# Performance work log

Measured on AMD Instinct MI355X. Metric: run time of the kernel, lower is better.

Reference implementation:

```python
import jax, jax.numpy as jnp
import numpy as np

EPS_PEN = 1e-05


def _penalty(x):
    return jnp.sqrt(x + EPS_PEN)


def _warp(img, flow):
    """Bilinear warp (Resample2d): sample img at (x+u, y+v), clamped borders.
    img: (B,C,H,W), flow: (B,2,H,W) -> (B,C,H,W)."""
    B, C, H, W = img.shape
    xs = jnp.arange(W, dtype=flow.dtype)[None, None, :]  # (1,1,W)
    ys = jnp.arange(H, dtype=flow.dtype)[None, :, None]  # (1,H,1)
    x = xs + flow[:, 0]  # (B,H,W)
    y = ys + flow[:, 1]
    x0f = jnp.floor(x)
    y0f = jnp.floor(y)
    wx = x - x0f  # bilinear weights
    wy = y - y0f
    x0 = jnp.clip(x0f.astype(jnp.int32), 0, W - 1)
    x1 = jnp.clip(x0 + 1, 0, W - 1)
    y0 = jnp.clip(y0f.astype(jnp.int32), 0, H - 1)
    y1 = jnp.clip(y0 + 1, 0, H - 1)
    img_flat = img.reshape(B, C, H * W)

    def gather(yi, xi):
        idx = (yi * W + xi).reshape(B, 1, H * W)
        idx = jnp.broadcast_to(idx, (B, C, H * W))
        return jnp.take_along_axis(img_flat, idx, axis=2).reshape(B, C, H, W)

    v00 = gather(y0, x0)
    v01 = gather(y0, x1)
    v10 = gather(y1, x0)
    v11 = gather(y1, x1)
    wx = wx[:, None]  # (B,1,H,W)
    wy = wy[:, None]
    return ((1 - wy) * ((1 - wx) * v00 + wx * v01)
            + wy * ((1 - wx) * v10 + wx * v11))


def _energy(flow, img1, img2, alpha=1.0, beta=1.0):
    img2_warp = _warp(img2, flow)
    A = jnp.sum((img1 - img2_warp) ** 2, axis=1)          # (B,H,W)
    data_term = jnp.sum(_penalty(A), axis=(1, 2))          # (B,)
    # conv with kernel_dx == horizontal forward diff per channel; dy vertical
    dx = flow[:, :, :, 1:] - flow[:, :, :, :-1]            # (B,2,H,W-1)
    dy = flow[:, :, 1:, :] - flow[:, :, :-1, :]            # (B,2,H-1,W)
    Bx = jnp.pad(jnp.sum(dx ** 2, axis=1), ((0, 0), (0, 0), (0, 1)))
    By = jnp.pad(jnp.sum(dy ** 2, axis=1), ((0, 0), (0, 1), (0, 0)))
    smooth_term = jnp.sum(_penalty(Bx + By), axis=(1, 2))  # (B,)
    return alpha * data_term + beta * smooth_term


def setup_inputs() -> dict:
    key = jax.random.key(0)
    ks = jax.random.split(key, 6)
    B, H, W = 16, 448, 1024
    mean = jax.random.normal(ks[0], (B, 2, H, W), dtype=jnp.float32)
    log_var = jax.random.normal(ks[1], (B, 2, H, W), dtype=jnp.float32)
    img1 = jax.random.uniform(ks[2], (B, 3, H, W), dtype=jnp.float32)
    img2 = jax.random.uniform(ks[3], (B, 3, H, W), dtype=jnp.float32)
    target = jax.random.normal(ks[4], (B, 2, H, W), dtype=jnp.float32)
    eps = jax.random.normal(ks[5], (B, 2, H, W), dtype=jnp.float32)
    return {"mean": mean, "log_var": log_var, "img1": img1, "img2": img2,
            "target": target, "eps": eps}


def reference(mean, log_var, img1, img2, target, eps):
    # reparam: z = mean + exp(log_var/2) * eps  (eps replaces Normal(0,1).sample)
    flow_sample = mean + jnp.exp(log_var / 2.0) * eps
    elbo = _energy(flow_sample, img1, img2) - jnp.sum(log_var, axis=(1, 2, 3)) / 2.0
    mean_elbo = jnp.mean(elbo)
    # elementwise EPE: L2 norm over flow channels of (mean - target)
    epe = jnp.sqrt(jnp.sum((mean - target) ** 2, axis=1))
    mean_epe = jnp.mean(epe)
    return (mean_elbo, mean_epe)
```

## Files before the change

### kernel.cpp

```cpp
#include <hip/hip_runtime.h>

#define BB 16
#define HH 448
#define WW 1024
constexpr int HW    = HH * WW;
constexpr int NBLK  = BB * HH;
constexpr int NTHR  = 256;
constexpr long long TOTAL = (long long)BB * HW;


struct FlowRaw {
    float m0, m1, l0, l1, e0, e1;
    float dm0, dm1, dl0, dl1, de0, de1;
    float t0, t1;
};

__global__ __launch_bounds__(NTHR) void elbo_main(
    const float* __restrict__ mean, const float* __restrict__ lvar,
    const float* __restrict__ img1, const float* __restrict__ img2,
    const float* __restrict__ target, const float* __restrict__ eps,
    float2* __restrict__ partials)
{
    constexpr int NXCD = 8, CPX = NBLK / NXCD;
    const int wg = (blockIdx.x % NXCD) * CPX + blockIdx.x / NXCD;

    const int b = wg / HH;
    const int y = wg - b * HH;
    const int t = threadIdx.x;

    const int fbase = b * 2 * HW + y * WW;
    const int ibase = b * 3 * HW;
    const bool have_dn = (y + 1) < HH;

    const float* __restrict__ p2c0 = img2 + ibase;
    const float* __restrict__ p2c1 = img2 + ibase + HW;
    const float* __restrict__ p2c2 = img2 + ibase + 2 * HW;

    float se = 0.f;
    float sp = 0.f;

    auto load_raw = [&](int k, FlowRaw& r) {
        const int o = fbase + (k << 8) + t;
        r.m0 = mean[o];   r.m1 = mean[o + HW];
        r.l0 = lvar[o];   r.l1 = lvar[o + HW];
        r.e0 = eps[o];    r.e1 = eps[o + HW];
        r.t0 = target[o]; r.t1 = target[o + HW];
        if (have_dn) {
            r.dm0 = mean[o + WW]; r.dm1 = mean[o + WW + HW];
            r.dl0 = lvar[o + WW]; r.dl1 = lvar[o + WW + HW];
            r.de0 = eps[o + WW];  r.de1 = eps[o + WW + HW];
        } else {
            r.dm0 = r.dm1 = r.dl0 = r.dl1 = r.de0 = r.de1 = 0.f;
        }
    };

    FlowRaw cur, nxt;
    load_raw(0, cur);

    #pragma unroll
    for (int k = 0; k < 4; ++k) {
        if (k < 3) load_raw(k + 1, nxt);

        const int x = (k << 8) + t;
        const int o = fbase + x;

        const float u = cur.m0 + __expf(0.5f * cur.l0) * cur.e0;
        const float v = cur.m1 + __expf(0.5f * cur.l1) * cur.e1;
        float un = 0.f, vn = 0.f;
        if (have_dn) {
            un = cur.dm0 + __expf(0.5f * cur.dl0) * cur.de0;
            vn = cur.dm1 + __expf(0.5f * cur.dl1) * cur.de1;
        }

        {
            const float du = cur.m0 - cur.t0, dv = cur.m1 - cur.t1;
            sp += sqrtf(du * du + dv * dv);
        }
        se -= 0.5f * (cur.l0 + cur.l1);

        float uR = __shfl_down(u, 1);
        float vR = __shfl_down(v, 1);
        if (((t & 63) == 63) && (x + 1 < WW)) {
            const int o1 = o + 1;
            uR = mean[o1]      + __expf(0.5f * lvar[o1])      * eps[o1];
            vR = mean[o1 + HW] + __expf(0.5f * lvar[o1 + HW]) * eps[o1 + HW];
        }

        float dx2 = 0.f, dy2 = 0.f;
        if (x < WW - 1) { const float a = uR - u, c = vR - v; dx2 = a * a + c * c; }
        if (have_dn)    { const float a = un - u, c = vn - v; dy2 = a * a + c * c; }
        se += sqrtf(dx2 + dy2 + 1e-5f);

        const float xs = (float)x + u;
        const float ys = (float)y + v;
        const float x0f = floorf(xs), y0f = floorf(ys);
        const float wx = xs - x0f,    wy = ys - y0f;
        int x0 = (int)x0f; x0 = min(max(x0, 0), WW - 1);
        const int x1 = min(x0 + 1, WW - 1);
        int yy0 = (int)y0f; yy0 = min(max(yy0, 0), HH - 1);
        const int yy1 = min(yy0 + 1, HH - 1);
        const int i00 = yy0 * WW + x0, i01 = yy0 * WW + x1;
        const int i10 = yy1 * WW + x0, i11 = yy1 * WW + x1;

        const int ro = y * WW + x;
        const float i1a = img1[ibase + ro];
        const float i1b = img1[ibase + HW + ro];
        const float i1c = img1[ibase + 2 * HW + ro];

        const float a00 = p2c0[i00], a01 = p2c0[i01], a10 = p2c0[i10], a11 = p2c0[i11];
        const float b00 = p2c1[i00], b01 = p2c1[i01], b10 = p2c1[i10], b11 = p2c1[i11];
        const float c00 = p2c2[i00], c01 = p2c2[i01], c10 = p2c2[i10], c11 = p2c2[i11];

        float A = 0.f;
        {
            const float top = a00 + wx * (a01 - a00);
            const float bot = a10 + wx * (a11 - a10);
            const float w   = top + wy * (bot - top);
            const float d   = i1a - w;  A += d * d;
        }
        {
            const float top = b00 + wx * (b01 - b00);
            const float bot = b10 + wx * (b11 - b10);
            const float w   = top + wy * (bot - top);
            const float d   = i1b - w;  A += d * d;
        }
        {
            const float top = c00 + wx * (c01 - c00);
            const float bot = c10 + wx * (c11 - c10);
            const float w   = top + wy * (bot - top);
            const float d   = i1c - w;  A += d * d;
        }
        se += sqrtf(A + 1e-5f);

        if (k < 3) cur = nxt;
    }

    #pragma unroll
    for (int off = 32; off > 0; off >>= 1) {
        se += __shfl_down(se, off);
        sp += __shfl_down(sp, off);
    }
    __shared__ float s_e[NTHR / 64], s_p[NTHR / 64];
    const int lane = threadIdx.x & 63;
    const int wid  = threadIdx.x >> 6;
    if (lane == 0) { s_e[wid] = se; s_p[wid] = sp; }
    __syncthreads();
    if (threadIdx.x == 0) {
        float te = 0.0f, tp = 0.0f;
        #pragma unroll
        for (int i = 0; i < NTHR / 64; ++i) { te += s_e[i]; tp += s_p[i]; }
        partials[blockIdx.x] = make_float2(te, tp);
    }
}

__global__ __launch_bounds__(256) void elbo_final(
    const float2* __restrict__ partials, float* __restrict__ out)
{
    double se = 0.0, sp = 0.0;
    for (int i = threadIdx.x; i < NBLK; i += 256) {
        const float2 v = partials[i];
        se += (double)v.x;
        sp += (double)v.y;
    }
    #pragma unroll
    for (int off = 32; off > 0; off >>= 1) {
        se += __shfl_down(se, off);
        sp += __shfl_down(sp, off);
    }
    __shared__ double s_e[4], s_p[4];
    const int lane = threadIdx.x & 63;
    const int wid  = threadIdx.x >> 6;
    if (lane == 0) { s_e[wid] = se; s_p[wid] = sp; }
    __syncthreads();
    if (threadIdx.x == 0) {
        double te = 0.0, tp = 0.0;
        #pragma unroll
        for (int i = 0; i < 4; ++i) { te += s_e[i]; tp += s_p[i]; }
        out[0] = (float)(te / (double)BB);
        out[1] = (float)(tp / (double)TOTAL);
    }
}

extern "C" void kernel_launch(void* const* d_in, const int* in_sizes, int n_in,
                              void* d_out, int out_size, void* d_ws, size_t ws_size,
                              hipStream_t stream) {
    const float* mean   = (const float*)d_in[0];
    const float* logvar = (const float*)d_in[1];
    const float* img1   = (const float*)d_in[2];
    const float* img2   = (const float*)d_in[3];
    const float* target = (const float*)d_in[4];
    const float* eps    = (const float*)d_in[5];
    float* out = (float*)d_out;
    float2* partials = (float2*)d_ws;

    elbo_main<<<NBLK, NTHR, 0, stream>>>(mean, logvar, img1, img2, target, eps, partials);
    elbo_final<<<1, 256, 0, stream>>>(partials, out);
}
```

Baseline: 404.5 us.

## Batch all loads per thread up front and widen final reduction to 1024 threads

Restructures the main kernel so every thread issues all flow, log-variance, eps, target, down-row and img1 loads for its four columns before any compute, then issues all 48 bilinear gathers before blending. The aim is more memory-level parallelism, replacing the one-step software prefetch. The final reduction now runs with 1024 threads, each doing a fixed unrolled set of partial loads. The cost is much higher register pressure (the gather array alone is 48 floats), which could cut occupancy or cause spills.

```diff
diff --git a/kernel.cpp b/kernel.cpp
--- a/kernel.cpp
+++ b/kernel.cpp
@@ -8,12 +8,6 @@
 constexpr int NTHR  = 256;
 constexpr long long TOTAL = (long long)BB * HW;
 
-
-struct FlowRaw {
-    float m0, m1, l0, l1, e0, e1;
-    float dm0, dm1, dl0, dl1, de0, de1;
-    float t0, t1;
-};
 
 __global__ __launch_bounds__(NTHR) void elbo_main(
     const float* __restrict__ mean, const float* __restrict__ lvar,
@@ -39,100 +33,105 @@
     float se = 0.f;
     float sp = 0.f;
 
-    auto load_raw = [&](int k, FlowRaw& r) {
+    float m0[4], m1[4], l0[4], l1[4], e0[4], e1[4], t0[4], t1[4];
+    float dm0[4], dm1[4], dl0[4], dl1[4], de0[4], de1[4];
+    float i1a[4], i1b[4], i1c[4];
+    #pragma unroll
+    for (int k = 0; k < 4; ++k) {
         const int o = fbase + (k << 8) + t;
-        r.m0 = mean[o];   r.m1 = mean[o + HW];
-        r.l0 = lvar[o];   r.l1 = lvar[o + HW];
-        r.e0 = eps[o];    r.e1 = eps[o + HW];
-        r.t0 = target[o]; r.t1 = target[o + HW];
-        if (have_dn) {
-            r.dm0 = mean[o + WW]; r.dm1 = mean[o + WW + HW];
-            r.dl0 = lvar[o + WW]; r.dl1 = lvar[o + WW + HW];
-            r.de0 = eps[o + WW];  r.de1 = eps[o + WW + HW];
-        } else {
-            r.dm0 = r.dm1 = r.dl0 = r.dl1 = r.de0 = r.de1 = 0.f;
-        }
-    };
-
-    FlowRaw cur, nxt;
-    load_raw(0, cur);
-
-    #pragma unroll
-    for (int k = 0; k < 4; ++k) {
-        if (k < 3) load_raw(k + 1, nxt);
-
+        m0[k] = mean[o];   m1[k] = mean[o + HW];
+        l0[k] = lvar[o];   l1[k] = lvar[o + HW];
+        e0[k] = eps[o];    e1[k] = eps[o + HW];
+        t0[k] = target[o]; t1[k] = target[o + HW];
+    }
+    if (have_dn) {
+        #pragma unroll
+        for (int k = 0; k < 4; ++k) {
+            const int o = fbase + WW + (k << 8) + t;
+            dm0[k] = mean[o]; dm1[k] = mean[o + HW];
+            dl0[k] = lvar[o]; dl1[k] = lvar[o + HW];
+            de0[k] = eps[o];  de1[k] = eps[o + HW];
+        }
+    }
+    #pragma unroll
+    for (int k = 0; k < 4; ++k) {
+        const int ro = y * WW + (k << 8) + t;
+        i1a[k] = img1[ibase + ro];
+        i1b[k] = img1[ibase + HW + ro];
+        i1c[k] = img1[ibase + 2 * HW + ro];
+    }
+
+    float u[4], v[4];
+    #pragma unroll
+    for (int k = 0; k < 4; ++k) {
+        u[k] = m0[k] + __expf(0.5f * l0[k]) * e0[k];
+        v[k] = m1[k] + __expf(0.5f * l1[k]) * e1[k];
+        const float du = m0[k] - t0[k], dv = m1[k] - t1[k];
+        sp += sqrtf(du * du + dv * dv);
+        se -= 0.5f * (l0[k] + l1[k]);
+    }
+    #pragma unroll
+    for (int k = 0; k < 4; ++k) {
         const int x = (k << 8) + t;
-        const int o = fbase + x;
-
-        const float u = cur.m0 + __expf(0.5f * cur.l0) * cur.e0;
-        const float v = cur.m1 + __expf(0.5f * cur.l1) * cur.e1;
-        float un = 0.f, vn = 0.f;
-        if (have_dn) {
-            un = cur.dm0 + __expf(0.5f * cur.dl0) * cur.de0;
-            vn = cur.dm1 + __expf(0.5f * cur.dl1) * cur.de1;
-        }
-
-        {
-            const float du = cur.m0 - cur.t0, dv = cur.m1 - cur.t1;
-            sp += sqrtf(du * du + dv * dv);
-        }
-        se -= 0.5f * (cur.l0 + cur.l1);
-
-        float uR = __shfl_down(u, 1);
-        float vR = __shfl_down(v, 1);
+        float uR = __shfl_down(u[k], 1);
+        float vR = __shfl_down(v[k], 1);
         if (((t & 63) == 63) && (x + 1 < WW)) {
-            const int o1 = o + 1;
+            const int o1 = fbase + x + 1;
             uR = mean[o1]      + __expf(0.5f * lvar[o1])      * eps[o1];
             vR = mean[o1 + HW] + __expf(0.5f * lvar[o1 + HW]) * eps[o1 + HW];
         }
-
         float dx2 = 0.f, dy2 = 0.f;
-        if (x < WW - 1) { const float a = uR - u, c = vR - v; dx2 = a * a + c * c; }
-        if (have_dn)    { const float a = un - u, c = vn - v; dy2 = a * a + c * c; }
+        if (x < WW - 1) { const float a = uR - u[k], c = vR - v[k]; dx2 = a * a + c * c; }
+        if (have_dn) {
+            const float un = dm0[k] + __expf(0.5f * dl0[k]) * de0[k];
+            const float vn = dm1[k] + __expf(0.5f * dl1[k]) * de1[k];
+            const float a = un - u[k], c = vn - v[k]; dy2 = a * a + c * c;
+        }
         se += sqrtf(dx2 + dy2 + 1e-5f);
-
-        const float xs = (float)x + u;
-        const float ys = (float)y + v;
+    }
+
+    float g[4][12], wxv[4], wyv[4];
+    #pragma unroll
+    for (int k = 0; k < 4; ++k) {
+        const int x = (k << 8) + t;
+        const float xs = (float)x + u[k];
+        const float ys = (float)y + v[k];
         const float x0f = floorf(xs), y0f = floorf(ys);
-        const float wx = xs - x0f,    wy = ys - y0f;
+        wxv[k] = xs - x0f; wyv[k] = ys - y0f;
         int x0 = (int)x0f; x0 = min(max(x0, 0), WW - 1);
         const int x1 = min(x0 + 1, WW - 1);
         int yy0 = (int)y0f; yy0 = min(max(yy0, 0), HH - 1);
         const int yy1 = min(yy0 + 1, HH - 1);
         const int i00 = yy0 * WW + x0, i01 = yy0 * WW + x1;
         const int i10 = yy1 * WW + x0, i11 = yy1 * WW + x1;
-
-        const int ro = y * WW + x;
-        const float i1a = img1[ibase + ro];
-        const float i1b = img1[ibase + HW + ro];
-        const float i1c = img1[ibase + 2 * HW + ro];
-
-        const float a00 = p2c0[i00], a01 = p2c0[i01], a10 = p2c0[i10], a11 = p2c0[i11];
-        const float b00 = p2c1[i00], b01 = p2c1[i01], b10 = p2c1[i10], b11 = p2c1[i11];
-        const float c00 = p2c2[i00], c01 = p2c2[i01], c10 = p2c2[i10], c11 = p2c2[i11];
-
+        g[k][0] = p2c0[i00]; g[k][1]  = p2c0[i01]; g[k][2]  = p2c0[i10]; g[k][3]  = p2c0[i11];
+        g[k][4] = p2c1[i00]; g[k][5]  = p2c1[i01]; g[k][6]  = p2c1[i10]; g[k][7]  = p2c1[i11];
+        g[k][8] = p2c2[i00]; g[k][9]  = p2c2[i01]; g[k][10] = p2c2[i10]; g[k][11] = p2c2[i11];
+    }
+
+    #pragma unroll
+    for (int k = 0; k < 4; ++k) {
+        const float wx = wxv[k], wy = wyv[k];
         float A = 0.f;
         {
-            const float top = a00 + wx * (a01 - a00);
-            const float bot = a10 + wx * (a11 - a10);
+            const float top = g[k][0] + wx * (g[k][1] - g[k][0]);
+            const float bot = g[k][2] + wx * (g[k][3] - g[k][2]);
             const float w   = top + wy * (bot - top);
-            const float d   = i1a - w;  A += d * d;
+            const float d   = i1a[k] - w;  A += d * d;
         }
         {
-            const float top = b00 + wx * (b01 - b00);
-            const float bot = b10 + wx * (b11 - b10);
+            const float top = g[k][4] + wx * (g[k][5] - g[k][4]);
+            const float bot = g[k][6] + wx * (g[k][7] - g[k][6]);
             const float w   = top + wy * (bot - top);
-            const float d   = i1b - w;  A += d * d;
+            const float d   = i1b[k] - w;  A += d * d;
         }
         {
-            const float top = c00 + wx * (c01 - c00);
-            const float bot = c10 + wx * (c11 - c10);
+            const float top = g[k][8] + wx * (g[k][9] - g[k][8]);
+            const float bot = g[k][10] + wx * (g[k][11] - g[k][10]);
             const float w   = top + wy * (bot - top);
-            const float d   = i1c - w;  A += d * d;
+            const float d   = i1c[k] - w;  A += d * d;
         }
         se += sqrtf(A + 1e-5f);
-
-        if (k < 3) cur = nxt;
     }
 
     #pragma unroll
@@ -153,21 +152,24 @@
     }
 }
 
-__global__ __launch_bounds__(256) void elbo_final(
+__global__ __launch_bounds__(1024) void elbo_final(
     const float2* __restrict__ partials, float* __restrict__ out)
 {
+    constexpr int PER = NBLK / 1024;
+    float2 v[PER];
+    #pragma unroll
+    for (int j = 0; j < PER; ++j) v[j] = partials[threadIdx.x + j * 1024];
+
     double se = 0.0, sp = 0.0;
-    for (int i = threadIdx.x; i < NBLK; i += 256) {
-        const float2 v = partials[i];
-        se += (double)v.x;
-        sp += (double)v.y;
-    }
+    #pragma unroll
+    for (int j = 0; j < PER; ++j) { se += (double)v[j].x; sp += (double)v[j].y; }
+
     #pragma unroll
     for (int off = 32; off > 0; off >>= 1) {
         se += __shfl_down(se, off);
         sp += __shfl_down(sp, off);
     }
-    __shared__ double s_e[4], s_p[4];
+    __shared__ double s_e[16], s_p[16];
     const int lane = threadIdx.x & 63;
     const int wid  = threadIdx.x >> 6;
     if (lane == 0) { s_e[wid] = se; s_p[wid] = sp; }
@@ -175,7 +177,7 @@
     if (threadIdx.x == 0) {
         double te = 0.0, tp = 0.0;
         #pragma unroll
-        for (int i = 0; i < 4; ++i) { te += s_e[i]; tp += s_p[i]; }
+        for (int i = 0; i < 16; ++i) { te += s_e[i]; tp += s_p[i]; }
         out[0] = (float)(te / (double)BB);
         out[1] = (float)(tp / (double)TOTAL);
     }
@@ -194,5 +196,5 @@
     float2* partials = (float2*)d_ws;
 
     elbo_main<<<NBLK, NTHR, 0, stream>>>(mean, logvar, img1, img2, target, eps, partials);
-    elbo_final<<<1, 256, 0, stream>>>(partials, out);
+    elbo_final<<<1, 1024, 0, stream>>>(partials, out);
 }
```

Result: faster. 392.2 us (-3.0%).
